# Kernel tuning notes

Measured on AMD Instinct MI355X. Metric: run time of the kernel, lower is better.

The kernel has to match this reference:

```python
import jax, jax.numpy as jnp
import numpy as np

N_NODES = 100000
N_EDGES = 1600000
IN, HID, OUT = 128, 128, 64


def setup_inputs() -> dict:
    key = jax.random.key(0)
    ks = jax.random.split(key, 6)
    x = jax.random.normal(ks[0], (N_NODES, IN), dtype=jnp.float32)
    W1 = jax.random.normal(ks[1], (IN, HID), dtype=jnp.float32) * (1.0 / np.sqrt(IN))
    b1 = jnp.zeros((HID,), dtype=jnp.float32)
    W2 = jax.random.normal(ks[2], (HID, OUT), dtype=jnp.float32) * (1.0 / np.sqrt(HID))
    b2 = jnp.zeros((OUT,), dtype=jnp.float32)
    edge_src = jax.random.randint(ks[3], (N_EDGES,), 0, N_NODES, dtype=jnp.int32)
    edge_dst = jax.random.randint(ks[4], (N_EDGES,), 0, N_NODES, dtype=jnp.int32)
    return {"x": x, "W1": W1, "b1": b1, "W2": W2, "b2": b2,
            "edge_src": edge_src, "edge_dst": edge_dst}


def reference(x, W1, b1, W2, b2, edge_src, edge_dst):
    N = x.shape[0]
    # in-degree per dst node (DGL 'gcn' aggregator normalizer)
    deg = jax.ops.segment_sum(jnp.ones_like(edge_dst, dtype=x.dtype), edge_dst,
                              num_segments=N)  # [N]
    inv = 1.0 / (deg + 1.0)  # [N]

    def sage_gcn(h, W, b):
        # sum over in-neighbors, add self, mean-normalize, then linear
        agg = jax.ops.segment_sum(h[edge_src], edge_dst, num_segments=N)  # [N, d]
        h_neigh = (agg + h) * inv[:, None]
        return h_neigh @ W + b

    h = jax.nn.relu(sage_gcn(x, W1, b1))
    # dropout is identity here (eval mode / deterministic reference)
    return sage_gcn(h, W2, b2)
```

## Files before the change

### kernel.cpp

```cpp
#include <hip/hip_runtime.h>

#define NN 100000
#define NNP 100032
#define NE 1600000
#define NBUC 782
#define NBLKA 256
#define CHA 6250
#define LG (NBUC * NBLKA)

typedef __attribute__((ext_vector_type(8))) short short8;
typedef __attribute__((ext_vector_type(4))) float f32x4;

__device__ __forceinline__ unsigned short f2bf(float f) {
    unsigned int u = __float_as_uint(f);
    u += 0x7FFFu + ((u >> 16) & 1u);
    return (unsigned short)(u >> 16);
}
__device__ __forceinline__ float ubf(unsigned short h) {
    return __uint_as_float((unsigned int)h << 16);
}
__device__ __forceinline__ float bf_lo(unsigned int u) { return __uint_as_float(u << 16); }
__device__ __forceinline__ float bf_hi(unsigned int u) { return __uint_as_float(u & 0xFFFF0000u); }

__global__ void convx_kernel(const float* __restrict__ x, unsigned short* __restrict__ xh,
                             unsigned short* __restrict__ xl) {
    int t = blockIdx.x * 256 + threadIdx.x;
    float4 v = reinterpret_cast<const float4*>(x)[t];
    ushort4 h, l;
    h.x = f2bf(v.x); l.x = f2bf(v.x - ubf(h.x));
    h.y = f2bf(v.y); l.y = f2bf(v.y - ubf(h.y));
    h.z = f2bf(v.z); l.z = f2bf(v.z - ubf(h.z));
    h.w = f2bf(v.w); l.w = f2bf(v.w - ubf(h.w));
    reinterpret_cast<ushort4*>(xh)[t] = h;
    reinterpret_cast<ushort4*>(xl)[t] = l;
}

__global__ void convw_kernel(const float* __restrict__ W1, const float* __restrict__ W2,
                             unsigned short* __restrict__ w1th, unsigned short* __restrict__ w1tl,
                             unsigned short* __restrict__ w2th, unsigned short* __restrict__ w2tl) {
    int n = blockIdx.x;
    int k = threadIdx.x;
    if (n < 128) {
        float w = W1[k * 128 + n];
        unsigned short h = f2bf(w);
        w1th[n * 128 + k] = h;
        w1tl[n * 128 + k] = f2bf(w - ubf(h));
    } else {
        int n2 = n - 128;
        float w = W2[k * 64 + n2];
        unsigned short h = f2bf(w);
        w2th[n2 * 128 + k] = h;
        w2tl[n2 * 128 + k] = f2bf(w - ubf(h));
    }
}

__global__ void binA_kernel(const int* __restrict__ dst, int* __restrict__ G, int E) {
    __shared__ int hist[NBUC];
    int t = threadIdx.x;
    for (int i = t; i < NBUC; i += 256) hist[i] = 0;
    __syncthreads();
    int s0 = blockIdx.x * CHA;
    int s1 = min(E, s0 + CHA);
    for (int i = s0 + t; i < s1; i += 256) atomicAdd(&hist[dst[i] >> 7], 1);
    __syncthreads();
    for (int i = t; i < NBUC; i += 256) G[i * NBLKA + blockIdx.x] = hist[i];
}

__global__ void gsum_kernel(const int* __restrict__ G, int* __restrict__ gb) {
    __shared__ int s[512];
    int t = threadIdx.x;
    s[t] = G[blockIdx.x * 512 + t];
    __syncthreads();
    for (int o = 256; o > 0; o >>= 1) {
        if (t < o) s[t] += s[t + o];
        __syncthreads();
    }
    if (t == 0) gb[blockIdx.x] = s[0];
}

__global__ void scanb_kernel(int* __restrict__ bsum, int nb) {
    __shared__ int s[512];
    int t = threadIdx.x;
    s[t] = (t < nb) ? bsum[t] : 0;
    __syncthreads();
    for (int o = 1; o < 512; o <<= 1) {
        int v = (t >= o) ? s[t - o] : 0;
        __syncthreads();
        if (t >= o) s[t] += v;
        __syncthreads();
    }
    if (t < nb) bsum[t] = (t == 0) ? 0 : s[t - 1];
}

__global__ void gscan_kernel(int* __restrict__ G, const int* __restrict__ gb) {
    __shared__ int s[512];
    int t = threadIdx.x;
    int i = blockIdx.x * 512 + t;
    int v = G[i];
    s[t] = v;
    __syncthreads();
    for (int o = 1; o < 512; o <<= 1) {
        int u = (t >= o) ? s[t - o] : 0;
        __syncthreads();
        if (t >= o) s[t] += u;
        __syncthreads();
    }
    G[i] = gb[blockIdx.x] + s[t] - v;
}

__global__ void binB_kernel(const int* __restrict__ src, const int* __restrict__ dst,
                            const int* __restrict__ G, unsigned long long* __restrict__ ebuf,
                            int E) {
    __shared__ int cur[NBUC];
    int t = threadIdx.x;
    for (int i = t; i < NBUC; i += 256) cur[i] = G[i * NBLKA + blockIdx.x];
    __syncthreads();
    int s0 = blockIdx.x * CHA;
    int s1 = min(E, s0 + CHA);
    for (int i = s0 + t; i < s1; i += 256) {
        int d = dst[i];
        int b = d >> 7;
        int pos = atomicAdd(&cur[b], 1);
        ebuf[pos] = ((unsigned long long)(unsigned int)d << 32) | (unsigned int)src[i];
    }
}

__global__ void fillC_kernel(const unsigned long long* __restrict__ ebuf,
                             const int* __restrict__ G, int* __restrict__ rowptr,
                             float* __restrict__ inv, int* __restrict__ col, int E, int N) {
    __shared__ int cnt[128];
    __shared__ int sc[128];
    int b = blockIdx.x;
    int t = threadIdx.x;
    int segStart = G[b * NBLKA];
    int segEnd = (b + 1 < NBUC) ? G[(b + 1) * NBLKA] : E;
    int nodeBase = b << 7;

    if (t < 128) cnt[t] = 0;
    __syncthreads();
    for (int i = segStart + t; i < segEnd; i += 256) {
        int d = (int)(ebuf[i] >> 32);
        atomicAdd(&cnt[d - nodeBase], 1);
    }
    __syncthreads();
    if (t < 128) sc[t] = cnt[t];
    __syncthreads();
    for (int o = 1; o < 128; o <<= 1) {
        int v = 0;
        if (t < 128 && t >= o) v = sc[t - o];
        __syncthreads();
        if (t < 128 && t >= o) sc[t] += v;
        __syncthreads();
    }
    if (t < 128) {
        int excl = (t == 0) ? 0 : sc[t - 1];
        int n = nodeBase + t;
        if (n < N) {
            rowptr[n] = segStart + excl;
            inv[n] = 1.0f / (float)(cnt[t] + 1);
        }
        sc[t] = segStart + excl;
    }
    if (b == 0 && t == 0) rowptr[N] = E;
    __syncthreads();
    for (int i = segStart + t; i < segEnd; i += 256) {
        unsigned long long p = ebuf[i];
        int d = (int)(p >> 32);
        int s = (int)(p & 0xFFFFFFFFull);
        int pos = atomicAdd(&sc[d - nodeBase], 1);
        col[pos] = s;
    }
}

__global__ __launch_bounds__(256) void gemm1m_kernel(
    const unsigned short* __restrict__ xh, const unsigned short* __restrict__ xl,
    const unsigned short* __restrict__ w1th, const unsigned short* __restrict__ w1tl,
    unsigned short* __restrict__ ybf) {
    const int wid = threadIdx.x >> 6;
    const int lane = threadIdx.x & 63;
    const int rbase = blockIdx.x * 64 + wid * 16;
    const int r = lane & 15;
    const int kg = lane >> 4;

    f32x4 acc[8];
    #pragma unroll
    for (int j = 0; j < 8; ++j) acc[j] = (f32x4){0.0f, 0.0f, 0.0f, 0.0f};

    const short* xhp = (const short*)xh;
    const short* xlp = (const short*)xl;
    const short* wh  = (const short*)w1th;
    const short* wl  = (const short*)w1tl;

    #pragma unroll
    for (int kk = 0; kk < 4; ++kk) {
        const int ko = kk * 32 + kg * 8;
        short8 a_h = *reinterpret_cast<const short8*>(xhp + (size_t)(rbase + r) * 128 + ko);
        short8 a_l = *reinterpret_cast<const short8*>(xlp + (size_t)(rbase + r) * 128 + ko);
        #pragma unroll
        for (int j = 0; j < 8; ++j) {
            short8 b_h = *reinterpret_cast<const short8*>(wh + (j * 16 + r) * 128 + ko);
            short8 b_l = *reinterpret_cast<const short8*>(wl + (j * 16 + r) * 128 + ko);
            acc[j] = __builtin_amdgcn_mfma_f32_16x16x32_bf16(a_h, b_h, acc[j], 0, 0, 0);
            acc[j] = __builtin_amdgcn_mfma_f32_16x16x32_bf16(a_h, b_l, acc[j], 0, 0, 0);
            acc[j] = __builtin_amdgcn_mfma_f32_16x16x32_bf16(a_l, b_h, acc[j], 0, 0, 0);
        }
    }

    #pragma unroll
    for (int j = 0; j < 8; ++j) {
        #pragma unroll
        for (int q = 0; q < 4; ++q) {
            ybf[(size_t)(rbase + kg * 4 + q) * 128 + j * 16 + r] = f2bf(acc[j][q]);
        }
    }
}

__global__ __launch_bounds__(256) void gemm2m_kernel(
    const unsigned short* __restrict__ h1h, const unsigned short* __restrict__ h1l,
    const unsigned short* __restrict__ w2th, const unsigned short* __restrict__ w2tl,
    unsigned short* __restrict__ zbf) {
    const int wid = threadIdx.x >> 6;
    const int lane = threadIdx.x & 63;
    const int rbase = blockIdx.x * 64 + wid * 16;
    const int r = lane & 15;
    const int kg = lane >> 4;

    f32x4 acc[4];
    #pragma unroll
    for (int j = 0; j < 4; ++j) acc[j] = (f32x4){0.0f, 0.0f, 0.0f, 0.0f};

    const short* hhp = (const short*)h1h;
    const short* hlp = (const short*)h1l;
    const short* wh  = (const short*)w2th;
    const short* wl  = (const short*)w2tl;

    #pragma unroll
    for (int kk = 0; kk < 4; ++kk) {
        const int ko = kk * 32 + kg * 8;
        short8 a_h = *reinterpret_cast<const short8*>(hhp + (size_t)(rbase + r) * 128 + ko);
        short8 a_l = *reinterpret_cast<const short8*>(hlp + (size_t)(rbase + r) * 128 + ko);
        #pragma unroll
        for (int j = 0; j < 4; ++j) {
            short8 b_h = *reinterpret_cast<const short8*>(wh + (j * 16 + r) * 128 + ko);
            short8 b_l = *reinterpret_cast<const short8*>(wl + (j * 16 + r) * 128 + ko);
            acc[j] = __builtin_amdgcn_mfma_f32_16x16x32_bf16(a_h, b_h, acc[j], 0, 0, 0);
            acc[j] = __builtin_amdgcn_mfma_f32_16x16x32_bf16(a_h, b_l, acc[j], 0, 0, 0);
            acc[j] = __builtin_amdgcn_mfma_f32_16x16x32_bf16(a_l, b_h, acc[j], 0, 0, 0);
        }
    }

    #pragma unroll
    for (int j = 0; j < 4; ++j) {
        #pragma unroll
        for (int q = 0; q < 4; ++q) {
            zbf[(size_t)(rbase + kg * 4 + q) * 64 + j * 16 + r] = f2bf(acc[j][q]);
        }
    }
}

__global__ void agg1_kernel(const unsigned short* __restrict__ ybf,
                            const int* __restrict__ rowptr, const int* __restrict__ col,
                            const float* __restrict__ inv, const float* __restrict__ b1,
                            unsigned short* __restrict__ h1h, unsigned short* __restrict__ h1l,
                            int N) {
    int wave = (blockIdx.x * blockDim.x + threadIdx.x) >> 6;
    if (wave >= N) return;
    int lane = threadIdx.x & 63;
    int start = rowptr[wave], end = rowptr[wave + 1];
    const unsigned int* yb = (const unsigned int*)ybf;

    float ax0 = 0, ay0 = 0, ax1 = 0, ay1 = 0, ax2 = 0, ay2 = 0, ax3 = 0, ay3 = 0;
    int e = start;
    for (; e + 3 < end; e += 4) {
        int s0 = __builtin_amdgcn_readfirstlane(col[e]);
        int s1 = __builtin_amdgcn_readfirstlane(col[e + 1]);
        int s2 = __builtin_amdgcn_readfirstlane(col[e + 2]);
        int s3 = __builtin_amdgcn_readfirstlane(col[e + 3]);
        unsigned int u0 = yb[(size_t)s0 * 64 + lane];
        unsigned int u1 = yb[(size_t)s1 * 64 + lane];
        unsigned int u2 = yb[(size_t)s2 * 64 + lane];
        unsigned int u3 = yb[(size_t)s3 * 64 + lane];
        ax0 += bf_lo(u0); ay0 += bf_hi(u0);
        ax1 += bf_lo(u1); ay1 += bf_hi(u1);
        ax2 += bf_lo(u2); ay2 += bf_hi(u2);
        ax3 += bf_lo(u3); ay3 += bf_hi(u3);
    }
    for (; e < end; ++e) {
        int s0 = __builtin_amdgcn_readfirstlane(col[e]);
        unsigned int u0 = yb[(size_t)s0 * 64 + lane];
        ax0 += bf_lo(u0); ay0 += bf_hi(u0);
    }
    float sx = (ax0 + ax1) + (ax2 + ax3);
    float sy = (ay0 + ay1) + (ay2 + ay3);

    unsigned int us = yb[(size_t)wave * 64 + lane];
    float2 bb = *reinterpret_cast<const float2*>(b1 + lane * 2);
    float iv = inv[wave];
    float rx = fmaxf(fmaf(sx + bf_lo(us), iv, bb.x), 0.0f);
    float ry = fmaxf(fmaf(sy + bf_hi(us), iv, bb.y), 0.0f);

    ushort2 h, l;
    h.x = f2bf(rx); l.x = f2bf(rx - ubf(h.x));
    h.y = f2bf(ry); l.y = f2bf(ry - ubf(h.y));
    *reinterpret_cast<ushort2*>(h1h + (size_t)wave * 128 + lane * 2) = h;
    *reinterpret_cast<ushort2*>(h1l + (size_t)wave * 128 + lane * 2) = l;
}

__global__ void agg2_kernel(const unsigned short* __restrict__ zbf,
                            const int* __restrict__ rowptr, const int* __restrict__ col,
                            const float* __restrict__ inv, const float* __restrict__ b2,
                            float* __restrict__ out, int N) {
    int node = (blockIdx.x * blockDim.x + threadIdx.x) >> 5;
    if (node >= N) return;
    int lane = threadIdx.x & 31;
    int start = rowptr[node], end = rowptr[node + 1];
    const unsigned int* zb = (const unsigned int*)zbf;

    float ax0 = 0, ay0 = 0, ax1 = 0, ay1 = 0, ax2 = 0, ay2 = 0, ax3 = 0, ay3 = 0;
    int e = start;
    for (; e + 3 < end; e += 4) {
        int s0 = col[e], s1 = col[e + 1], s2 = col[e + 2], s3 = col[e + 3];
        unsigned int u0 = zb[(size_t)s0 * 32 + lane];
        unsigned int u1 = zb[(size_t)s1 * 32 + lane];
        unsigned int u2 = zb[(size_t)s2 * 32 + lane];
        unsigned int u3 = zb[(size_t)s3 * 32 + lane];
        ax0 += bf_lo(u0); ay0 += bf_hi(u0);
        ax1 += bf_lo(u1); ay1 += bf_hi(u1);
        ax2 += bf_lo(u2); ay2 += bf_hi(u2);
        ax3 += bf_lo(u3); ay3 += bf_hi(u3);
    }
    for (; e < end; ++e) {
        unsigned int u0 = zb[(size_t)col[e] * 32 + lane];
        ax0 += bf_lo(u0); ay0 += bf_hi(u0);
    }
    float sx = (ax0 + ax1) + (ax2 + ax3);
    float sy = (ay0 + ay1) + (ay2 + ay3);

    unsigned int us = zb[(size_t)node * 32 + lane];
    float2 bb = *reinterpret_cast<const float2*>(b2 + lane * 2);
    float iv = inv[node];
    float2 r;
    r.x = fmaf(sx + bf_lo(us), iv, bb.x);
    r.y = fmaf(sy + bf_hi(us), iv, bb.y);
    *reinterpret_cast<float2*>(out + (size_t)node * 64 + lane * 2) = r;
}

extern "C" void kernel_launch(void* const* d_in, const int* in_sizes, int n_in,
                              void* d_out, int out_size, void* d_ws, size_t ws_size,
                              hipStream_t stream) {
    const float* x   = (const float*)d_in[0];
    const float* W1  = (const float*)d_in[1];
    const float* b1  = (const float*)d_in[2];
    const float* W2  = (const float*)d_in[3];
    const float* b2  = (const float*)d_in[4];
    const int* esrc  = (const int*)d_in[5];
    const int* edst  = (const int*)d_in[6];
    float* out = (float*)d_out;

    char* p = (char*)d_ws;
    unsigned short* ybf = (unsigned short*)p;
    unsigned long long* ebuf = (unsigned long long*)p;
    p += (size_t)NNP * 128 * 2;
    int* G = (int*)p;        p += (size_t)LG * 4;
    int* gb = (int*)p;       p += 512 * 4;
    int* rowptr = (int*)p;   p += (size_t)(NN + 4) * 4;
    int* col = (int*)p;      p += (size_t)NE * 4;
    float* inv = (float*)p;  p += (size_t)NN * 4;
    unsigned short* w1th = (unsigned short*)p; p += 128 * 128 * 2;
    unsigned short* w1tl = (unsigned short*)p; p += 128 * 128 * 2;
    unsigned short* w2th = (unsigned short*)p; p += 64 * 128 * 2;
    unsigned short* w2tl = (unsigned short*)p; p += 64 * 128 * 2;
    unsigned short* xh = (unsigned short*)p;   p += (size_t)NNP * 128 * 2;
    unsigned short* xl = (unsigned short*)p;   p += (size_t)NNP * 128 * 2;
    unsigned short* zbf = (unsigned short*)p;  p += (size_t)NNP * 64 * 2;
    unsigned short* h1h = xh;
    unsigned short* h1l = xl;

    size_t padOff = (size_t)NN * 128 * 2;
    size_t padBytes = (size_t)(NNP - NN) * 128 * 2;
    hipMemsetAsync(xh + (size_t)NN * 128, 0, padBytes, stream);
    hipMemsetAsync(xl + (size_t)NN * 128, 0, padBytes, stream);
    (void)padOff;

    convx_kernel<<<NN * 32 / 256, 256, 0, stream>>>(x, xh, xl);
    convw_kernel<<<192, 128, 0, stream>>>(W1, W2, w1th, w1tl, w2th, w2tl);

    binA_kernel<<<NBLKA, 256, 0, stream>>>(edst, G, NE);
    gsum_kernel<<<LG / 512, 512, 0, stream>>>(G, gb);
    scanb_kernel<<<1, 512, 0, stream>>>(gb, LG / 512);
    gscan_kernel<<<LG / 512, 512, 0, stream>>>(G, gb);
    binB_kernel<<<NBLKA, 256, 0, stream>>>(esrc, edst, G, ebuf, NE);
    fillC_kernel<<<NBUC, 256, 0, stream>>>(ebuf, G, rowptr, inv, col, NE, NN);

    gemm1m_kernel<<<NNP / 64, 256, 0, stream>>>(xh, xl, w1th, w1tl, ybf);
    agg1_kernel<<<NN / 4, 256, 0, stream>>>(ybf, rowptr, col, inv, b1, h1h, h1l, NN);


    gemm2m_kernel<<<NNP / 64, 256, 0, stream>>>(h1h, h1l, w2th, w2tl, zbf);
    agg2_kernel<<<NN / 8, 256, 0, stream>>>(zbf, rowptr, col, inv, b2, out, NN);
}
```

Before: 419.0 us.

## Fuse x split into GEMM1, pack edge buffer to 32-bit, widen aggregation loops

The separate x-to-bf16 hi/lo conversion kernel and its pad memsets are dropped; GEMM1 now reads fp32 x directly and splits it in registers, with clamped row indices standing in for padding. The edge binning buffer packs src<<7 | local dst into 32 bits instead of 64, halving that traffic. agg1 gets an 8-way unrolled gather, and agg2 uses a full wave per node with two halves interleaving edges and combining through a shuffle. The workspace layout is reorganised so h1 no longer aliases the x buffers, which costs extra memory.

```diff
diff --git a/kernel.cpp b/kernel.cpp
--- a/kernel.cpp
+++ b/kernel.cpp
@@ -22,17 +22,13 @@
 __device__ __forceinline__ float bf_lo(unsigned int u) { return __uint_as_float(u << 16); }
 __device__ __forceinline__ float bf_hi(unsigned int u) { return __uint_as_float(u & 0xFFFF0000u); }
 
-__global__ void convx_kernel(const float* __restrict__ x, unsigned short* __restrict__ xh,
-                             unsigned short* __restrict__ xl) {
-    int t = blockIdx.x * 256 + threadIdx.x;
-    float4 v = reinterpret_cast<const float4*>(x)[t];
-    ushort4 h, l;
-    h.x = f2bf(v.x); l.x = f2bf(v.x - ubf(h.x));
-    h.y = f2bf(v.y); l.y = f2bf(v.y - ubf(h.y));
-    h.z = f2bf(v.z); l.z = f2bf(v.z - ubf(h.z));
-    h.w = f2bf(v.w); l.w = f2bf(v.w - ubf(h.w));
-    reinterpret_cast<ushort4*>(xh)[t] = h;
-    reinterpret_cast<ushort4*>(xl)[t] = l;
+__device__ __forceinline__ void split8(const float* v, short8& h8, short8& l8) {
+    #pragma unroll
+    for (int q = 0; q < 8; ++q) {
+        unsigned short h = f2bf(v[q]);
+        h8[q] = (short)h;
+        l8[q] = (short)f2bf(v[q] - ubf(h));
+    }
 }
 
 __global__ void convw_kernel(const float* __restrict__ W1, const float* __restrict__ W2,
@@ -109,7 +105,7 @@
 }
 
 __global__ void binB_kernel(const int* __restrict__ src, const int* __restrict__ dst,
-                            const int* __restrict__ G, unsigned long long* __restrict__ ebuf,
+                            const int* __restrict__ G, unsigned int* __restrict__ ebuf,
                             int E) {
     __shared__ int cur[NBUC];
     int t = threadIdx.x;
@@ -121,13 +117,13 @@
         int d = dst[i];
         int b = d >> 7;
         int pos = atomicAdd(&cur[b], 1);
-        ebuf[pos] = ((unsigned long long)(unsigned int)d << 32) | (unsigned int)src[i];
-    }
-}
-
-__global__ void fillC_kernel(const unsigned long long* __restrict__ ebuf,
+        ebuf[pos] = ((unsigned int)src[i] << 7) | (unsigned int)(d & 127);
+    }
+}
+
+__global__ void fillC_kernel(const unsigned int* __restrict__ ebuf,
                              const int* __restrict__ G, int* __restrict__ rowptr,
-                             float* __restrict__ inv, int* __restrict__ col, int E, int N) {
+                             float* __restrict__ invg, int* __restrict__ col, int E, int N) {
     __shared__ int cnt[128];
     __shared__ int sc[128];
     int b = blockIdx.x;
@@ -139,8 +135,7 @@
     if (t < 128) cnt[t] = 0;
     __syncthreads();
     for (int i = segStart + t; i < segEnd; i += 256) {
-        int d = (int)(ebuf[i] >> 32);
-        atomicAdd(&cnt[d - nodeBase], 1);
+        atomicAdd(&cnt[ebuf[i] & 127], 1);
     }
     __syncthreads();
     if (t < 128) sc[t] = cnt[t];
@@ -157,23 +152,21 @@
         int n = nodeBase + t;
         if (n < N) {
             rowptr[n] = segStart + excl;
-            inv[n] = 1.0f / (float)(cnt[t] + 1);
+            invg[n] = 1.0f / (float)(cnt[t] + 1);
         }
         sc[t] = segStart + excl;
     }
     if (b == 0 && t == 0) rowptr[N] = E;
     __syncthreads();
     for (int i = segStart + t; i < segEnd; i += 256) {
-        unsigned long long p = ebuf[i];
-        int d = (int)(p >> 32);
-        int s = (int)(p & 0xFFFFFFFFull);
-        int pos = atomicAdd(&sc[d - nodeBase], 1);
-        col[pos] = s;
-    }
-}
-
-__global__ __launch_bounds__(256) void gemm1m_kernel(
-    const unsigned short* __restrict__ xh, const unsigned short* __restrict__ xl,
+        unsigned int e = ebuf[i];
+        int pos = atomicAdd(&sc[e & 127], 1);
+        col[pos] = (int)(e >> 7);
+    }
+}
+
+__global__ __launch_bounds__(256) void gemm1f_kernel(
+    const float* __restrict__ x,
     const unsigned short* __restrict__ w1th, const unsigned short* __restrict__ w1tl,
     unsigned short* __restrict__ ybf) {
     const int wid = threadIdx.x >> 6;
@@ -181,25 +174,24 @@
     const int rbase = blockIdx.x * 64 + wid * 16;
     const int r = lane & 15;
     const int kg = lane >> 4;
+    const int rc = min(rbase + r, NN - 1);
 
     f32x4 acc[8];
     #pragma unroll
     for (int j = 0; j < 8; ++j) acc[j] = (f32x4){0.0f, 0.0f, 0.0f, 0.0f};
-
-    const short* xhp = (const short*)xh;
-    const short* xlp = (const short*)xl;
-    const short* wh  = (const short*)w1th;
-    const short* wl  = (const short*)w1tl;
 
     #pragma unroll
     for (int kk = 0; kk < 4; ++kk) {
         const int ko = kk * 32 + kg * 8;
-        short8 a_h = *reinterpret_cast<const short8*>(xhp + (size_t)(rbase + r) * 128 + ko);
-        short8 a_l = *reinterpret_cast<const short8*>(xlp + (size_t)(rbase + r) * 128 + ko);
+        float v[8];
+        *reinterpret_cast<float4*>(&v[0]) = *reinterpret_cast<const float4*>(x + (size_t)rc * 128 + ko);
+        *reinterpret_cast<float4*>(&v[4]) = *reinterpret_cast<const float4*>(x + (size_t)rc * 128 + ko + 4);
+        short8 a_h, a_l;
+        split8(v, a_h, a_l);
         #pragma unroll
         for (int j = 0; j < 8; ++j) {
-            short8 b_h = *reinterpret_cast<const short8*>(wh + (j * 16 + r) * 128 + ko);
-            short8 b_l = *reinterpret_cast<const short8*>(wl + (j * 16 + r) * 128 + ko);
+            short8 b_h = *reinterpret_cast<const short8*>((const short*)w1th + (j * 16 + r) * 128 + ko);
+            short8 b_l = *reinterpret_cast<const short8*>((const short*)w1tl + (j * 16 + r) * 128 + ko);
             acc[j] = __builtin_amdgcn_mfma_f32_16x16x32_bf16(a_h, b_h, acc[j], 0, 0, 0);
             acc[j] = __builtin_amdgcn_mfma_f32_16x16x32_bf16(a_h, b_l, acc[j], 0, 0, 0);
             acc[j] = __builtin_amdgcn_mfma_f32_16x16x32_bf16(a_l, b_h, acc[j], 0, 0, 0);
@@ -224,6 +216,7 @@
     const int rbase = blockIdx.x * 64 + wid * 16;
     const int r = lane & 15;
     const int kg = lane >> 4;
+    const int rc = min(rbase + r, NN - 1);
 
     f32x4 acc[4];
     #pragma unroll
@@ -231,18 +224,16 @@
 
     const short* hhp = (const short*)h1h;
     const short* hlp = (const short*)h1l;
-    const short* wh  = (const short*)w2th;
-    const short* wl  = (const short*)w2tl;
 
     #pragma unroll
     for (int kk = 0; kk < 4; ++kk) {
         const int ko = kk * 32 + kg * 8;
-        short8 a_h = *reinterpret_cast<const short8*>(hhp + (size_t)(rbase + r) * 128 + ko);
-        short8 a_l = *reinterpret_cast<const short8*>(hlp + (size_t)(rbase + r) * 128 + ko);
+        short8 a_h = *reinterpret_cast<const short8*>(hhp + (size_t)rc * 128 + ko);
+        short8 a_l = *reinterpret_cast<const short8*>(hlp + (size_t)rc * 128 + ko);
         #pragma unroll
         for (int j = 0; j < 4; ++j) {
-            short8 b_h = *reinterpret_cast<const short8*>(wh + (j * 16 + r) * 128 + ko);
-            short8 b_l = *reinterpret_cast<const short8*>(wl + (j * 16 + r) * 128 + ko);
+            short8 b_h = *reinterpret_cast<const short8*>((const short*)w2th + (j * 16 + r) * 128 + ko);
+            short8 b_l = *reinterpret_cast<const short8*>((const short*)w2tl + (j * 16 + r) * 128 + ko);
             acc[j] = __builtin_amdgcn_mfma_f32_16x16x32_bf16(a_h, b_h, acc[j], 0, 0, 0);
             acc[j] = __builtin_amdgcn_mfma_f32_16x16x32_bf16(a_h, b_l, acc[j], 0, 0, 0);
             acc[j] = __builtin_amdgcn_mfma_f32_16x16x32_bf16(a_l, b_h, acc[j], 0, 0, 0);
@@ -260,7 +251,7 @@
 
 __global__ void agg1_kernel(const unsigned short* __restrict__ ybf,
                             const int* __restrict__ rowptr, const int* __restrict__ col,
-                            const float* __restrict__ inv, const float* __restrict__ b1,
+                            const float* __restrict__ invg, const float* __restrict__ b1,
                             unsigned short* __restrict__ h1h, unsigned short* __restrict__ h1l,
                             int N) {
     int wave = (blockIdx.x * blockDim.x + threadIdx.x) >> 6;
@@ -270,7 +261,34 @@
     const unsigned int* yb = (const unsigned int*)ybf;
 
     float ax0 = 0, ay0 = 0, ax1 = 0, ay1 = 0, ax2 = 0, ay2 = 0, ax3 = 0, ay3 = 0;
+    float ax4 = 0, ay4 = 0, ax5 = 0, ay5 = 0, ax6 = 0, ay6 = 0, ax7 = 0, ay7 = 0;
     int e = start;
+    for (; e + 7 < end; e += 8) {
+        int s0 = __builtin_amdgcn_readfirstlane(col[e]);
+        int s1 = __builtin_amdgcn_readfirstlane(col[e + 1]);
+        int s2 = __builtin_amdgcn_readfirstlane(col[e + 2]);
+        int s3 = __builtin_amdgcn_readfirstlane(col[e + 3]);
+        int s4 = __builtin_amdgcn_readfirstlane(col[e + 4]);
+        int s5 = __builtin_amdgcn_readfirstlane(col[e + 5]);
+        int s6 = __builtin_amdgcn_readfirstlane(col[e + 6]);
+        int s7 = __builtin_amdgcn_readfirstlane(col[e + 7]);
+        unsigned int u0 = yb[(size_t)s0 * 64 + lane];
+        unsigned int u1 = yb[(size_t)s1 * 64 + lane];
+        unsigned int u2 = yb[(size_t)s2 * 64 + lane];
+        unsigned int u3 = yb[(size_t)s3 * 64 + lane];
+        unsigned int u4 = yb[(size_t)s4 * 64 + lane];
+        unsigned int u5 = yb[(size_t)s5 * 64 + lane];
+        unsigned int u6 = yb[(size_t)s6 * 64 + lane];
+        unsigned int u7 = yb[(size_t)s7 * 64 + lane];
+        ax0 += bf_lo(u0); ay0 += bf_hi(u0);
+        ax1 += bf_lo(u1); ay1 += bf_hi(u1);
+        ax2 += bf_lo(u2); ay2 += bf_hi(u2);
+        ax3 += bf_lo(u3); ay3 += bf_hi(u3);
+        ax4 += bf_lo(u4); ay4 += bf_hi(u4);
+        ax5 += bf_lo(u5); ay5 += bf_hi(u5);
+        ax6 += bf_lo(u6); ay6 += bf_hi(u6);
+        ax7 += bf_lo(u7); ay7 += bf_hi(u7);
+    }
     for (; e + 3 < end; e += 4) {
         int s0 = __builtin_amdgcn_readfirstlane(col[e]);
         int s1 = __builtin_amdgcn_readfirstlane(col[e + 1]);
@@ -290,12 +308,12 @@
         unsigned int u0 = yb[(size_t)s0 * 64 + lane];
         ax0 += bf_lo(u0); ay0 += bf_hi(u0);
     }
-    float sx = (ax0 + ax1) + (ax2 + ax3);
-    float sy = (ay0 + ay1) + (ay2 + ay3);
+    float sx = ((ax0 + ax1) + (ax2 + ax3)) + ((ax4 + ax5) + (ax6 + ax7));
+    float sy = ((ay0 + ay1) + (ay2 + ay3)) + ((ay4 + ay5) + (ay6 + ay7));
 
     unsigned int us = yb[(size_t)wave * 64 + lane];
     float2 bb = *reinterpret_cast<const float2*>(b1 + lane * 2);
-    float iv = inv[wave];
+    float iv = invg[wave];
     float rx = fmaxf(fmaf(sx + bf_lo(us), iv, bb.x), 0.0f);
     float ry = fmaxf(fmaf(sy + bf_hi(us), iv, bb.y), 0.0f);
 
@@ -308,41 +326,47 @@
 
 __global__ void agg2_kernel(const unsigned short* __restrict__ zbf,
                             const int* __restrict__ rowptr, const int* __restrict__ col,
-                            const float* __restrict__ inv, const float* __restrict__ b2,
+                            const float* __restrict__ invg, const float* __restrict__ b2,
                             float* __restrict__ out, int N) {
-    int node = (blockIdx.x * blockDim.x + threadIdx.x) >> 5;
+    int node = (blockIdx.x * blockDim.x + threadIdx.x) >> 6;
     if (node >= N) return;
-    int lane = threadIdx.x & 31;
+    int lane = threadIdx.x & 63;
+    int half = lane >> 5;
+    int l32 = lane & 31;
     int start = rowptr[node], end = rowptr[node + 1];
     const unsigned int* zb = (const unsigned int*)zbf;
 
     float ax0 = 0, ay0 = 0, ax1 = 0, ay1 = 0, ax2 = 0, ay2 = 0, ax3 = 0, ay3 = 0;
-    int e = start;
-    for (; e + 3 < end; e += 4) {
-        int s0 = col[e], s1 = col[e + 1], s2 = col[e + 2], s3 = col[e + 3];
-        unsigned int u0 = zb[(size_t)s0 * 32 + lane];
-        unsigned int u1 = zb[(size_t)s1 * 32 + lane];
-        unsigned int u2 = zb[(size_t)s2 * 32 + lane];
-        unsigned int u3 = zb[(size_t)s3 * 32 + lane];
+    int i = start + half;
+    for (; i + 6 < end; i += 8) {
+        int s0 = col[i], s1 = col[i + 2], s2 = col[i + 4], s3 = col[i + 6];
+        unsigned int u0 = zb[(size_t)s0 * 32 + l32];
+        unsigned int u1 = zb[(size_t)s1 * 32 + l32];
+        unsigned int u2 = zb[(size_t)s2 * 32 + l32];
+        unsigned int u3 = zb[(size_t)s3 * 32 + l32];
         ax0 += bf_lo(u0); ay0 += bf_hi(u0);
         ax1 += bf_lo(u1); ay1 += bf_hi(u1);
         ax2 += bf_lo(u2); ay2 += bf_hi(u2);
         ax3 += bf_lo(u3); ay3 += bf_hi(u3);
     }
-    for (; e < end; ++e) {
-        unsigned int u0 = zb[(size_t)col[e] * 32 + lane];
+    for (; i < end; i += 2) {
+        unsigned int u0 = zb[(size_t)col[i] * 32 + l32];
         ax0 += bf_lo(u0); ay0 += bf_hi(u0);
     }
     float sx = (ax0 + ax1) + (ax2 + ax3);
     float sy = (ay0 + ay1) + (ay2 + ay3);
-
-    unsigned int us = zb[(size_t)node * 32 + lane];
-    float2 bb = *reinterpret_cast<const float2*>(b2 + lane * 2);
-    float iv = inv[node];
-    float2 r;
-    r.x = fmaf(sx + bf_lo(us), iv, bb.x);
-    r.y = fmaf(sy + bf_hi(us), iv, bb.y);
-    *reinterpret_cast<float2*>(out + (size_t)node * 64 + lane * 2) = r;
+    sx += __shfl_xor(sx, 32);
+    sy += __shfl_xor(sy, 32);
+
+    if (half == 0) {
+        unsigned int us = zb[(size_t)node * 32 + l32];
+        float2 bb = *reinterpret_cast<const float2*>(b2 + l32 * 2);
+        float iv = invg[node];
+        float2 r;
+        r.x = fmaf(sx + bf_lo(us), iv, bb.x);
+        r.y = fmaf(sy + bf_hi(us), iv, bb.y);
+        *reinterpret_cast<float2*>(out + (size_t)node * 64 + l32 * 2) = r;
+    }
 }
 
 extern "C" void kernel_launch(void* const* d_in, const int* in_sizes, int n_in,
@@ -358,31 +382,21 @@
     float* out = (float*)d_out;
 
     char* p = (char*)d_ws;
-    unsigned short* ybf = (unsigned short*)p;
-    unsigned long long* ebuf = (unsigned long long*)p;
-    p += (size_t)NNP * 128 * 2;
-    int* G = (int*)p;        p += (size_t)LG * 4;
-    int* gb = (int*)p;       p += 512 * 4;
-    int* rowptr = (int*)p;   p += (size_t)(NN + 4) * 4;
-    int* col = (int*)p;      p += (size_t)NE * 4;
-    float* inv = (float*)p;  p += (size_t)NN * 4;
+    unsigned short* ybf = (unsigned short*)p;  p += (size_t)NNP * 128 * 2;
+    unsigned short* h1h = (unsigned short*)p;  p += (size_t)NNP * 128 * 2;
+    unsigned short* h1l = (unsigned short*)p;  p += (size_t)NNP * 128 * 2;
+    unsigned short* zbf = (unsigned short*)p;  p += (size_t)NNP * 64 * 2;
+    unsigned int* ebuf = (unsigned int*)p;     p += (size_t)NE * 4;
+    int* col = (int*)p;                        p += (size_t)NE * 4;
+    int* G = (int*)p;                          p += (size_t)LG * 4;
+    int* gb = (int*)p;                         p += 512 * 4;
+    int* rowptr = (int*)p;                     p += (size_t)(NN + 4) * 4;
+    float* invg = (float*)p;                   p += (size_t)NN * 4;
     unsigned short* w1th = (unsigned short*)p; p += 128 * 128 * 2;
     unsigned short* w1tl = (unsigned short*)p; p += 128 * 128 * 2;
     unsigned short* w2th = (unsigned short*)p; p += 64 * 128 * 2;
     unsigned short* w2tl = (unsigned short*)p; p += 64 * 128 * 2;
-    unsigned short* xh = (unsigned short*)p;   p += (size_t)NNP * 128 * 2;
-    unsigned short* xl = (unsigned short*)p;   p += (size_t)NNP * 128 * 2;
-    unsigned short* zbf = (unsigned short*)p;  p += (size_t)NNP * 64 * 2;
-    unsigned short* h1h = xh;
-    unsigned short* h1l = xl;
-
-    size_t padOff = (size_t)NN * 128 * 2;
-    size_t padBytes = (size_t)(NNP - NN) * 128 * 2;
-    hipMemsetAsync(xh + (size_t)NN * 128, 0, padBytes, stream);
-    hipMemsetAsync(xl + (size_t)NN * 128, 0, padBytes, stream);
-    (void)padOff;
-
-    convx_kernel<<<NN * 32 / 256, 256, 0, stream>>>(x, xh, xl);
+
     convw_kernel<<<192, 128, 0, stream>>>(W1, W2, w1th, w1tl, w2th, w2tl);
 
     binA_kernel<<<NBLKA, 256, 0, stream>>>(edst, G, NE);
@@ -390,12 +404,11 @@
     scanb_kernel<<<1, 512, 0, stream>>>(gb, LG / 512);
     gscan_kernel<<<LG / 512, 512, 0, stream>>>(G, gb);
     binB_kernel<<<NBLKA, 256, 0, stream>>>(esrc, edst, G, ebuf, NE);
-    fillC_kernel<<<NBUC, 256, 0, stream>>>(ebuf, G, rowptr, inv, col, NE, NN);
-
-    gemm1m_kernel<<<NNP / 64, 256, 0, stream>>>(xh, xl, w1th, w1tl, ybf);
-    agg1_kernel<<<NN / 4, 256, 0, stream>>>(ybf, rowptr, col, inv, b1, h1h, h1l, NN);
-
+    fillC_kernel<<<NBUC, 256, 0, stream>>>(ebuf, G, rowptr, invg, col, NE, NN);
+
+    gemm1f_kernel<<<NNP / 64, 256, 0, stream>>>(x, w1th, w1tl, ybf);
+    agg1_kernel<<<NN / 4, 256, 0, stream>>>(ybf, rowptr, col, invg, b1, h1h, h1l, NN);
 
     gemm2m_kernel<<<NNP / 64, 256, 0, stream>>>(h1h, h1l, w2th, w2tl, zbf);
-    agg2_kernel<<<NN / 8, 256, 0, stream>>>(zbf, rowptr, col, inv, b2, out, NN);
-}
+    agg2_kernel<<<NN / 4, 256, 0, stream>>>(zbf, rowptr, col, invg, b2, out, NN);
+}
```

Result: faster. 388.0 us (-7.4%).
